# Performance work log

Measured on AMD Instinct MI355X. Metric: run time of the kernel, lower is better.

The kernel has to match this reference:

```python
import jax, jax.numpy as jnp
import numpy as np
from jax import lax

STRIDE = 2
PADDING = 2
KERNEL = 5


def _conv_transpose3d(x, weight, bias):
    # weight: [C_in, C_out, kd, kh, kw] (PyTorch ConvTranspose3d layout)
    # Equivalent dense conv: flip kernel spatially, swap in/out channels,
    # lhs_dilation=stride, symmetric padding = dilation*(k-1) - padding.
    w_t = jnp.flip(weight, axis=(2, 3, 4)).transpose(1, 0, 2, 3, 4)  # [C_out, C_in, k,k,k]
    pad = KERNEL - 1 - PADDING  # = 2
    y = lax.conv_general_dilated(
        x, w_t,
        window_strides=(1, 1, 1),
        padding=[(pad, pad)] * 3,
        lhs_dilation=(STRIDE, STRIDE, STRIDE),
        dimension_numbers=("NCDHW", "OIDHW", "NCDHW"),
    )
    return y + bias[None, :, None, None, None]


def _maxpool3d(y, k):
    # PyTorch MaxPool3d(kernel=k) -> stride=k, no padding, floor mode == VALID
    win = (1, 1, k, k, k)
    return lax.reduce_window(y, -jnp.inf, lax.max, win, win, "VALID")


def setup_inputs() -> dict:
    key = jax.random.key(0)
    k1, k2, k3 = jax.random.split(key, 3)
    x = jax.random.normal(k1, (16, 32, 16, 32, 32), dtype=jnp.float32)
    weight = jax.random.normal(k2, (32, 64, 5, 5, 5), dtype=jnp.float32) * 0.05
    bias = jax.random.normal(k3, (64,), dtype=jnp.float32) * 0.05
    return {"x": x, "weight": weight, "bias": bias}


def reference(x, weight, bias):
    y = _conv_transpose3d(x, weight, bias)     # [16, 64, 31, 63, 63]
    y = _maxpool3d(y, 2)                       # [16, 64, 15, 31, 31]
    y = _maxpool3d(y, 3)                       # [16, 64, 5, 10, 10]
    return jnp.sum(y, axis=1, keepdims=True)   # [16, 1, 5, 10, 10]
```

## Files before the change

### kernel.cpp

```cpp
#include <hip/hip_runtime.h>
#include <hip/hip_bf16.h>
#include <math.h>

typedef short bf16x8 __attribute__((ext_vector_type(8)));
typedef float f32x4 __attribute__((ext_vector_type(4)));

constexpr int CIN = 32, COUT = 64, D = 16, H = 32, W = 32;

constexpr size_t WS_NEED = 884736u;

static __device__ const unsigned char IT_CODE[24] = {
    0, 8, 16, 3,
    1, 9, 17, 11, 19, 7,
    2, 10, 18, 5, 13, 21, 15,
    4, 12, 20, 6, 14, 22, 23};
static __device__ const unsigned char IT_START[5] = {0, 4, 10, 17, 24};
static __device__ const unsigned char EPI_START[10] = {0, 1, 3, 5, 6, 7, 9, 11, 12, 13};
static __device__ const unsigned char EPI_CNT[10]   = {1, 2, 2, 1, 1, 2, 2, 1, 1, 2};

__global__ void prep_w(const float* __restrict__ w, unsigned short* __restrict__ wtp) {
    int idx = blockIdx.x * 256 + threadIdx.x;
    int ci  = idx & 31;
    int co  = (idx >> 5) & 63;
    int tt  = idx >> 11;
    int t   = tt % 27, cls = tt / 27;
    int td = t / 9, th = (t / 3) % 3, tw = t % 3;
    int pd = (cls >> 2) & 1, ph = (cls >> 1) & 1, pw = cls & 1;
    int kd = pd + 2 * td, kh = ph + 2 * th, kw = pw + 2 * tw;
    float v = 0.f;
    if (kd < 5 && kh < 5 && kw < 5)
        v = w[(ci * COUT + co) * 125 + kd * 25 + kh * 5 + kw];
    __hip_bfloat16 b = __float2bfloat16(v);
    wtp[idx] = *reinterpret_cast<unsigned short*>(&b);
}

__device__ __forceinline__ int lpA(int wrow, int quad) {
    return wrow * 64 + ((quad ^ ((wrow >> 1) & 3)) << 4);
}

__global__ __launch_bounds__(256, 2) void main_k(
    const unsigned short* __restrict__ wtp, const float* __restrict__ x,
    const float* __restrict__ bias, float* __restrict__ out)
{
    __shared__ unsigned short Xs[25600];
    int bx = blockIdx.x;
    int h0 = bx % 10;
    int d0 = (bx / 10) % 5;
    int n  = bx / 50;
    int tid = threadIdx.x;

    int id0 = 3 * d0 - 1, ih0 = 3 * h0 - 1;
    for (int u = tid; u < 6400; u += 256) {
        int q  = u & 7;
        int ci = (u >> 3) & 31;
        int p  = u >> 8;
        int dd = p / 5, hl = p % 5;
        int id = id0 + dd, ih = ih0 + hl;
        float4 v = {0.f, 0.f, 0.f, 0.f};
        if (id >= 0 && ih >= 0)
            v = ((const float4*)(x + (((size_t)(n * CIN + ci) * D + id) * H + ih) * W))[q];
        unsigned short hj[4];
        {
            __hip_bfloat16 b0 = __float2bfloat16(v.x); hj[0] = *reinterpret_cast<unsigned short*>(&b0);
            __hip_bfloat16 b1 = __float2bfloat16(v.y); hj[1] = *reinterpret_cast<unsigned short*>(&b1);
            __hip_bfloat16 b2 = __float2bfloat16(v.z); hj[2] = *reinterpret_cast<unsigned short*>(&b2);
            __hip_bfloat16 b3 = __float2bfloat16(v.w); hj[3] = *reinterpret_cast<unsigned short*>(&b3);
        }
        int rowb = p * 1024;
        int cig = ci >> 3, cil = ci & 7;
#pragma unroll
        for (int j = 0; j < 4; ++j) {
            int ww = 4 * q + 1 + j;
            if (ww < 32)
                Xs[rowb + ww * 32 + ((cig ^ ((ww >> 1) & 3)) << 3) + cil] = hj[j];
        }
        if (q == 0)
            Xs[rowb + (cig << 3) + cil] = 0;
    }

    int lane = tid & 63, wv = tid >> 6;
    int l15 = lane & 15, quad = lane >> 4;
    int wv_s = __builtin_amdgcn_readfirstlane(wv);

    int laneB = l15 * 64 + quad * 16;
    int m1 = 16 + l15; if (m1 > 29) m1 = 29;
    int lp00 = lpA(l15 + 0, quad), lp01 = lpA(l15 + 1, quad), lp02 = lpA(l15 + 2, quad);
    int lp10 = lpA(m1 + 0, quad),  lp11 = lpA(m1 + 1, quad),  lp12 = lpA(m1 + 2, quad);

    f32x4 mx[2][4];
#pragma unroll
    for (int mt = 0; mt < 2; ++mt)
#pragma unroll
        for (int nt = 0; nt < 4; ++nt) mx[mt][nt] = (f32x4){-INFINITY, -INFINITY, -INFINITY, -INFINITY};

    __syncthreads();
    const char* xsb = (const char*)Xs;

    int it0 = IT_START[wv_s], it1 = IT_START[wv_s + 1];
#pragma unroll 1
    for (int ii = it0; ii < it1; ++ii) {
        int code  = __builtin_amdgcn_readfirstlane(IT_CODE[ii]);
        int cls   = code & 7;
        int alpha = code >> 3;
        int ntd = 3 - ((cls >> 2) & 1), nth = 3 - ((cls >> 1) & 1), ntw = 3 - (cls & 1);
        const char* tbb = (const char*)wtp + (size_t)cls * 27 * 4096 + laneB;
        const int T = ntd * nth * ntw;

        f32x4 acc[3][2][4];
#pragma unroll
        for (int b = 0; b < 3; ++b)
#pragma unroll
            for (int mt = 0; mt < 2; ++mt)
#pragma unroll
                for (int nt = 0; nt < 4; ++nt) acc[b][mt][nt] = (f32x4){0.f, 0.f, 0.f, 0.f};

        int ptd = 0, pth = 0, ptw = 0;
        auto adv = [&]() {
            ++ptw;
            if (ptw == ntw) { ptw = 0; ++pth; if (pth == nth) { pth = 0; ++ptd; } }
        };

        bf16x8 bE0, bE1, bE2, bE3, aE0, aE1, aE2, aE3, aE4, aE5;
        {
            int Qb = ((alpha + 2) * 5 + 2) * 2048;
            bE0 = *(const bf16x8*)(tbb);
            bE1 = *(const bf16x8*)(tbb + 1024);
            bE2 = *(const bf16x8*)(tbb + 2048);
            bE3 = *(const bf16x8*)(tbb + 3072);
            const char* rb = xsb + Qb;
            aE0 = *(const bf16x8*)(rb + lp02);
            aE1 = *(const bf16x8*)(rb + lp12);
            aE2 = *(const bf16x8*)(rb + 2048 + lp02);
            aE3 = *(const bf16x8*)(rb + 2048 + lp12);
            aE4 = *(const bf16x8*)(rb + 4096 + lp02);
            aE5 = *(const bf16x8*)(rb + 4096 + lp12);
        }
        adv();
        bf16x8 bO0, bO1, bO2, bO3, aO0, aO1, aO2, aO3, aO4, aO5;
        {
            int Qb = ((alpha + 2 - ptd) * 5 + (2 - pth)) * 2048;
            int ss = 2 - ptw;
            const char* bq = tbb + (ptd * 9 + pth * 3 + ptw) * 4096;
            bO0 = *(const bf16x8*)(bq);
            bO1 = *(const bf16x8*)(bq + 1024);
            bO2 = *(const bf16x8*)(bq + 2048);
            bO3 = *(const bf16x8*)(bq + 3072);
            int lpa = ss == 0 ? lp00 : (ss == 1 ? lp01 : lp02);
            int lpb = ss == 0 ? lp10 : (ss == 1 ? lp11 : lp12);
            const char* rb = xsb + Qb;
            aO0 = *(const bf16x8*)(rb + lpa);
            aO1 = *(const bf16x8*)(rb + lpb);
            aO2 = *(const bf16x8*)(rb + 2048 + lpa);
            aO3 = *(const bf16x8*)(rb + 2048 + lpb);
            aO4 = *(const bf16x8*)(rb + 4096 + lpa);
            aO5 = *(const bf16x8*)(rb + 4096 + lpb);
        }
        adv();

#pragma unroll 1
        for (int it = 0; it < T; it += 2) {
            acc[0][0][0] = __builtin_amdgcn_mfma_f32_16x16x32_bf16(aE0, bE0, acc[0][0][0], 0, 0, 0);
            acc[0][0][1] = __builtin_amdgcn_mfma_f32_16x16x32_bf16(aE0, bE1, acc[0][0][1], 0, 0, 0);
            acc[0][0][2] = __builtin_amdgcn_mfma_f32_16x16x32_bf16(aE0, bE2, acc[0][0][2], 0, 0, 0);
            acc[0][0][3] = __builtin_amdgcn_mfma_f32_16x16x32_bf16(aE0, bE3, acc[0][0][3], 0, 0, 0);
            acc[0][1][0] = __builtin_amdgcn_mfma_f32_16x16x32_bf16(aE1, bE0, acc[0][1][0], 0, 0, 0);
            acc[0][1][1] = __builtin_amdgcn_mfma_f32_16x16x32_bf16(aE1, bE1, acc[0][1][1], 0, 0, 0);
            acc[0][1][2] = __builtin_amdgcn_mfma_f32_16x16x32_bf16(aE1, bE2, acc[0][1][2], 0, 0, 0);
            acc[0][1][3] = __builtin_amdgcn_mfma_f32_16x16x32_bf16(aE1, bE3, acc[0][1][3], 0, 0, 0);
            acc[1][0][0] = __builtin_amdgcn_mfma_f32_16x16x32_bf16(aE2, bE0, acc[1][0][0], 0, 0, 0);
            acc[1][0][1] = __builtin_amdgcn_mfma_f32_16x16x32_bf16(aE2, bE1, acc[1][0][1], 0, 0, 0);
            acc[1][0][2] = __builtin_amdgcn_mfma_f32_16x16x32_bf16(aE2, bE2, acc[1][0][2], 0, 0, 0);
            acc[1][0][3] = __builtin_amdgcn_mfma_f32_16x16x32_bf16(aE2, bE3, acc[1][0][3], 0, 0, 0);
            acc[1][1][0] = __builtin_amdgcn_mfma_f32_16x16x32_bf16(aE3, bE0, acc[1][1][0], 0, 0, 0);
            acc[1][1][1] = __builtin_amdgcn_mfma_f32_16x16x32_bf16(aE3, bE1, acc[1][1][1], 0, 0, 0);
            acc[1][1][2] = __builtin_amdgcn_mfma_f32_16x16x32_bf16(aE3, bE2, acc[1][1][2], 0, 0, 0);
            acc[1][1][3] = __builtin_amdgcn_mfma_f32_16x16x32_bf16(aE3, bE3, acc[1][1][3], 0, 0, 0);
            acc[2][0][0] = __builtin_amdgcn_mfma_f32_16x16x32_bf16(aE4, bE0, acc[2][0][0], 0, 0, 0);
            acc[2][0][1] = __builtin_amdgcn_mfma_f32_16x16x32_bf16(aE4, bE1, acc[2][0][1], 0, 0, 0);
            acc[2][0][2] = __builtin_amdgcn_mfma_f32_16x16x32_bf16(aE4, bE2, acc[2][0][2], 0, 0, 0);
            acc[2][0][3] = __builtin_amdgcn_mfma_f32_16x16x32_bf16(aE4, bE3, acc[2][0][3], 0, 0, 0);
            acc[2][1][0] = __builtin_amdgcn_mfma_f32_16x16x32_bf16(aE5, bE0, acc[2][1][0], 0, 0, 0);
            acc[2][1][1] = __builtin_amdgcn_mfma_f32_16x16x32_bf16(aE5, bE1, acc[2][1][1], 0, 0, 0);
            acc[2][1][2] = __builtin_amdgcn_mfma_f32_16x16x32_bf16(aE5, bE2, acc[2][1][2], 0, 0, 0);
            acc[2][1][3] = __builtin_amdgcn_mfma_f32_16x16x32_bf16(aE5, bE3, acc[2][1][3], 0, 0, 0);
            if (it + 2 < T) {
                int Qb = ((alpha + 2 - ptd) * 5 + (2 - pth)) * 2048;
                int ss = 2 - ptw;
                const char* bq = tbb + (ptd * 9 + pth * 3 + ptw) * 4096;
                bE0 = *(const bf16x8*)(bq);
                bE1 = *(const bf16x8*)(bq + 1024);
                bE2 = *(const bf16x8*)(bq + 2048);
                bE3 = *(const bf16x8*)(bq + 3072);
                int lpa = ss == 0 ? lp00 : (ss == 1 ? lp01 : lp02);
                int lpb = ss == 0 ? lp10 : (ss == 1 ? lp11 : lp12);
                const char* rb = xsb + Qb;
                aE0 = *(const bf16x8*)(rb + lpa);
                aE1 = *(const bf16x8*)(rb + lpb);
                aE2 = *(const bf16x8*)(rb + 2048 + lpa);
                aE3 = *(const bf16x8*)(rb + 2048 + lpb);
                aE4 = *(const bf16x8*)(rb + 4096 + lpa);
                aE5 = *(const bf16x8*)(rb + 4096 + lpb);
                adv();
            }
            if (it + 1 < T) {
                acc[0][0][0] = __builtin_amdgcn_mfma_f32_16x16x32_bf16(aO0, bO0, acc[0][0][0], 0, 0, 0);
                acc[0][0][1] = __builtin_amdgcn_mfma_f32_16x16x32_bf16(aO0, bO1, acc[0][0][1], 0, 0, 0);
                acc[0][0][2] = __builtin_amdgcn_mfma_f32_16x16x32_bf16(aO0, bO2, acc[0][0][2], 0, 0, 0);
                acc[0][0][3] = __builtin_amdgcn_mfma_f32_16x16x32_bf16(aO0, bO3, acc[0][0][3], 0, 0, 0);
                acc[0][1][0] = __builtin_amdgcn_mfma_f32_16x16x32_bf16(aO1, bO0, acc[0][1][0], 0, 0, 0);
                acc[0][1][1] = __builtin_amdgcn_mfma_f32_16x16x32_bf16(aO1, bO1, acc[0][1][1], 0, 0, 0);
                acc[0][1][2] = __builtin_amdgcn_mfma_f32_16x16x32_bf16(aO1, bO2, acc[0][1][2], 0, 0, 0);
                acc[0][1][3] = __builtin_amdgcn_mfma_f32_16x16x32_bf16(aO1, bO3, acc[0][1][3], 0, 0, 0);
                acc[1][0][0] = __builtin_amdgcn_mfma_f32_16x16x32_bf16(aO2, bO0, acc[1][0][0], 0, 0, 0);
                acc[1][0][1] = __builtin_amdgcn_mfma_f32_16x16x32_bf16(aO2, bO1, acc[1][0][1], 0, 0, 0);
                acc[1][0][2] = __builtin_amdgcn_mfma_f32_16x16x32_bf16(aO2, bO2, acc[1][0][2], 0, 0, 0);
                acc[1][0][3] = __builtin_amdgcn_mfma_f32_16x16x32_bf16(aO2, bO3, acc[1][0][3], 0, 0, 0);
                acc[1][1][0] = __builtin_amdgcn_mfma_f32_16x16x32_bf16(aO3, bO0, acc[1][1][0], 0, 0, 0);
                acc[1][1][1] = __builtin_amdgcn_mfma_f32_16x16x32_bf16(aO3, bO1, acc[1][1][1], 0, 0, 0);
                acc[1][1][2] = __builtin_amdgcn_mfma_f32_16x16x32_bf16(aO3, bO2, acc[1][1][2], 0, 0, 0);
                acc[1][1][3] = __builtin_amdgcn_mfma_f32_16x16x32_bf16(aO3, bO3, acc[1][1][3], 0, 0, 0);
                acc[2][0][0] = __builtin_amdgcn_mfma_f32_16x16x32_bf16(aO4, bO0, acc[2][0][0], 0, 0, 0);
                acc[2][0][1] = __builtin_amdgcn_mfma_f32_16x16x32_bf16(aO4, bO1, acc[2][0][1], 0, 0, 0);
                acc[2][0][2] = __builtin_amdgcn_mfma_f32_16x16x32_bf16(aO4, bO2, acc[2][0][2], 0, 0, 0);
                acc[2][0][3] = __builtin_amdgcn_mfma_f32_16x16x32_bf16(aO4, bO3, acc[2][0][3], 0, 0, 0);
                acc[2][1][0] = __builtin_amdgcn_mfma_f32_16x16x32_bf16(aO5, bO0, acc[2][1][0], 0, 0, 0);
                acc[2][1][1] = __builtin_amdgcn_mfma_f32_16x16x32_bf16(aO5, bO1, acc[2][1][1], 0, 0, 0);
                acc[2][1][2] = __builtin_amdgcn_mfma_f32_16x16x32_bf16(aO5, bO2, acc[2][1][2], 0, 0, 0);
                acc[2][1][3] = __builtin_amdgcn_mfma_f32_16x16x32_bf16(aO5, bO3, acc[2][1][3], 0, 0, 0);
                if (it + 3 < T) {
                    int Qb = ((alpha + 2 - ptd) * 5 + (2 - pth)) * 2048;
                    int ss = 2 - ptw;
                    const char* bq = tbb + (ptd * 9 + pth * 3 + ptw) * 4096;
                    bO0 = *(const bf16x8*)(bq);
                    bO1 = *(const bf16x8*)(bq + 1024);
                    bO2 = *(const bf16x8*)(bq + 2048);
                    bO3 = *(const bf16x8*)(bq + 3072);
                    int lpa = ss == 0 ? lp00 : (ss == 1 ? lp01 : lp02);
                    int lpb = ss == 0 ? lp10 : (ss == 1 ? lp11 : lp12);
                    const char* rb = xsb + Qb;
                    aO0 = *(const bf16x8*)(rb + lpa);
                    aO1 = *(const bf16x8*)(rb + lpb);
                    aO2 = *(const bf16x8*)(rb + 2048 + lpa);
                    aO3 = *(const bf16x8*)(rb + 2048 + lpb);
                    aO4 = *(const bf16x8*)(rb + 4096 + lpa);
                    aO5 = *(const bf16x8*)(rb + 4096 + lpb);
                    adv();
                }
            }
        }

#pragma unroll
        for (int mt = 0; mt < 2; ++mt)
#pragma unroll
            for (int nt = 0; nt < 4; ++nt)
#pragma unroll
                for (int r = 0; r < 4; ++r) {
                    float m = fmaxf(fmaxf(acc[0][mt][nt][r], acc[1][mt][nt][r]), acc[2][mt][nt][r]);
                    mx[mt][nt][r] = fmaxf(mx[mt][nt][r], m);
                }
    }

    __syncthreads();
    float* epi = (float*)Xs;
    int fsm0 = (0x3123 >> (quad * 4)) & 15;
    int fsm1 = (0x4312 >> (quad * 4)) & 15;
#pragma unroll
    for (int mt = 0; mt < 2; ++mt) {
        int fs = mt ? fsm1 : fsm0;
        int g  = mt * 4 + quad;
#pragma unroll
        for (int nt = 0; nt < 4; ++nt) {
            float a0 = mx[mt][nt][0], a1 = mx[mt][nt][1], a2 = mx[mt][nt][2], a3 = mx[mt][nt][3];
            float t01 = fmaxf(a0, a1), t012 = fmaxf(t01, a2), t0123 = fmaxf(t012, a3);
            float pA = fs == 1 ? a0 : (fs == 2 ? t01 : (fs == 3 ? t012 : t0123));
            float t23 = fmaxf(a2, a3), t123 = fmaxf(a1, t23);
            float pB = fs == 1 ? t123 : (fs == 2 ? t23 : (fs == 3 ? a3 : -INFINITY));
            epi[((wv * 8 + g) * 2 + 0) * 64 + nt * 16 + l15] = pA;
            epi[((wv * 8 + g) * 2 + 1) * 64 + nt * 16 + l15] = pB;
        }
    }
    __syncthreads();

    int elemBase = ((n * 5 + d0) * 10 + h0) * 10;
    float bco = bias[lane];
#pragma unroll 1
    for (int win = wv_s; win < 10; win += 4) {
        int st = EPI_START[win], cnt = EPI_CNT[win];
        float v = -INFINITY;
        for (int src = 0; src < 4; ++src)
            for (int e = st; e < st + cnt; ++e)
                v = fmaxf(v, epi[(src * 16 + e) * 64 + lane]);
        v += bco;
#pragma unroll
        for (int off = 32; off > 0; off >>= 1) v += __shfl_xor(v, off);
        if (lane == 0) out[elemBase + win] = v;
    }
}

__global__ __launch_bounds__(256) void fused_fallback(
    const float* __restrict__ x, const float* __restrict__ wsrc,
    const float* __restrict__ bias, float* __restrict__ out)
{
    __shared__ float xs[CIN * 125];
    __shared__ float wmax[4][64];
    const int b  = blockIdx.x;
    const int w0 = b % 10, h0 = (b / 10) % 10, d0 = (b / 100) % 5, n = b / 500;
    const int tid = threadIdx.x;
    const int id0 = 3 * d0 - 1, ih0 = 3 * h0 - 1, iw0 = 3 * w0 - 1;
    for (int e = tid; e < CIN * 125; e += 256) {
        int kk = e % 5, jj = (e / 5) % 5, ii = (e / 25) % 5, c = e / 125;
        int id = id0 + ii, ih = ih0 + jj, iw = iw0 + kk;
        float v = 0.f;
        if (id >= 0 && ih >= 0 && iw >= 0)
            v = x[(((n * CIN + c) * D + id) * H + ih) * W + iw];
        xs[e] = v;
    }
    __syncthreads();
    const int lane = tid & 63, wv = tid >> 6;
    float lmax = -INFINITY;
    for (int ccls = 0; ccls < 2; ++ccls) {
        const int cls = wv * 2 + ccls;
        const int pd = (cls >> 2) & 1, ph = (cls >> 1) & 1, pw = cls & 1;
        float acc[27];
#pragma unroll
        for (int i = 0; i < 27; ++i) acc[i] = 0.f;
        for (int ci = 0; ci < CIN; ++ci) {
            float wr[27];
#pragma unroll
            for (int t = 0; t < 27; ++t) {
                int td = t / 9, th = (t / 3) % 3, tw = t % 3;
                int kd = pd + 2 * td, kh = ph + 2 * th, kw = pw + 2 * tw;
                wr[t] = (kd < 5 && kh < 5 && kw < 5)
                          ? wsrc[((ci * 64 + lane) * 125) + kd * 25 + kh * 5 + kw] : 0.f;
            }
            const float* xb = xs + ci * 125;
#pragma unroll
            for (int td = 0; td < 3; ++td)
#pragma unroll
            for (int th = 0; th < 3; ++th)
#pragma unroll
            for (int tw = 0; tw < 3; ++tw) {
                const float wval = wr[(td * 3 + th) * 3 + tw];
#pragma unroll
                for (int a = 0; a < 3; ++a)
#pragma unroll
                for (int bb = 0; bb < 3; ++bb)
#pragma unroll
                for (int cc = 0; cc < 3; ++cc)
                    acc[(a * 3 + bb) * 3 + cc] +=
                        xb[(a + 2 - td) * 25 + (bb + 2 - th) * 5 + (cc + 2 - tw)] * wval;
            }
        }
#pragma unroll
        for (int i = 0; i < 27; ++i) lmax = fmaxf(lmax, acc[i]);
    }
    wmax[wv][lane] = lmax;
    __syncthreads();
    if (wv == 0) {
        float m = fmaxf(fmaxf(wmax[0][lane], wmax[1][lane]),
                        fmaxf(wmax[2][lane], wmax[3][lane]));
        m += bias[lane];
        for (int off = 32; off > 0; off >>= 1) m += __shfl_down(m, off);
        if (lane == 0) out[b] = m;
    }
}

extern "C" void kernel_launch(void* const* d_in, const int* in_sizes, int n_in,
                              void* d_out, int out_size, void* d_ws, size_t ws_size,
                              hipStream_t stream) {
    const float* x    = (const float*)d_in[0];
    const float* w    = (const float*)d_in[1];
    const float* bias = (const float*)d_in[2];
    float* out = (float*)d_out;

    if (ws_size >= WS_NEED) {
        unsigned short* wtp = (unsigned short*)d_ws;
        prep_w<<<1728, 256, 0, stream>>>(w, wtp);
        main_k<<<800, 256, 0, stream>>>(wtp, x, bias, out);
    } else {
        fused_fallback<<<8000, 256, 0, stream>>>(x, w, bias, out);
    }
}
```

Before: 201.7 us.

## Split each output row tile into two W-halves across blocks, raising occupancy

Each block now computes half of the output W range (one 16-row M tile instead of two), doubling the grid to 1600 blocks. Accumulator and A-fragment register use roughly halves, which allows launch bounds of 3 waves per SIMD, and the fold into partial pool windows moves into the per-iteration loop. It also adds s_setprio around MFMA bursts. The cost is reloading overlapping x halo and all weights per half-block, plus extra staging work.

Result: slower. 243.0 us (+20.5%).

```diff
diff --git a/kernel.cpp b/kernel.cpp
--- a/kernel.cpp
+++ b/kernel.cpp
@@ -15,8 +15,8 @@
     2, 10, 18, 5, 13, 21, 15,
     4, 12, 20, 6, 14, 22, 23};
 static __device__ const unsigned char IT_START[5] = {0, 4, 10, 17, 24};
-static __device__ const unsigned char EPI_START[10] = {0, 1, 3, 5, 6, 7, 9, 11, 12, 13};
-static __device__ const unsigned char EPI_CNT[10]   = {1, 2, 2, 1, 1, 2, 2, 1, 1, 2};
+static __device__ const unsigned char EPI_START[5] = {0, 1, 3, 5, 6};
+static __device__ const unsigned char EPI_CNT[5]   = {1, 2, 2, 1, 1};
 
 __global__ void prep_w(const float* __restrict__ w, unsigned short* __restrict__ wtp) {
     int idx = blockIdx.x * 256 + threadIdx.x;
@@ -38,22 +38,27 @@
     return wrow * 64 + ((quad ^ ((wrow >> 1) & 3)) << 4);
 }
 
-__global__ __launch_bounds__(256, 2) void main_k(
+__global__ __launch_bounds__(256, 3) void main_k(
     const unsigned short* __restrict__ wtp, const float* __restrict__ x,
     const float* __restrict__ bias, float* __restrict__ out)
 {
     __shared__ unsigned short Xs[25600];
-    int bx = blockIdx.x;
-    int h0 = bx % 10;
-    int d0 = (bx / 10) % 5;
-    int n  = bx / 50;
+    int bx   = blockIdx.x;
+    int half = bx & 1;
+    int obx  = bx >> 1;
+    int h0 = obx % 10;
+    int d0 = (obx / 10) % 5;
+    int n  = obx / 50;
     int tid = threadIdx.x;
 
     int id0 = 3 * d0 - 1, ih0 = 3 * h0 - 1;
-    for (int u = tid; u < 6400; u += 256) {
-        int q  = u & 7;
-        int ci = (u >> 3) & 31;
-        int p  = u >> 8;
+    int qb = half ? 3 : 0;
+    for (int u = tid; u < 4000; u += 256) {
+        int qi = u % 5;
+        int t2 = u / 5;
+        int ci = t2 & 31;
+        int p  = t2 >> 5;
+        int q  = qb + qi;
         int dd = p / 5, hl = p % 5;
         int id = id0 + dd, ih = ih0 + hl;
         float4 v = {0.f, 0.f, 0.f, 0.f};
@@ -83,18 +88,19 @@
     int wv_s = __builtin_amdgcn_readfirstlane(wv);
 
     int laneB = l15 * 64 + quad * 16;
-    int m1 = 16 + l15; if (m1 > 29) m1 = 29;
-    int lp00 = lpA(l15 + 0, quad), lp01 = lpA(l15 + 1, quad), lp02 = lpA(l15 + 2, quad);
-    int lp10 = lpA(m1 + 0, quad),  lp11 = lpA(m1 + 1, quad),  lp12 = lpA(m1 + 2, quad);
-
-    f32x4 mx[2][4];
-#pragma unroll
-    for (int mt = 0; mt < 2; ++mt)
-#pragma unroll
-        for (int nt = 0; nt < 4; ++nt) mx[mt][nt] = (f32x4){-INFINITY, -INFINITY, -INFINITY, -INFINITY};
+    int mtmp = 15 + l15;
+    int mb = half ? (mtmp > 29 ? 29 : mtmp) : l15;
+    int lp0 = lpA(mb + 0, quad), lp1 = lpA(mb + 1, quad), lp2 = lpA(mb + 2, quad);
+
+    float mxp[4][2];
+#pragma unroll
+    for (int nt = 0; nt < 4; ++nt) { mxp[nt][0] = -INFINITY; mxp[nt][1] = -INFINITY; }
 
     __syncthreads();
     const char* xsb = (const char*)Xs;
+
+    int fsm = half ? 0x4123 : 0x3123;
+    int fs  = (fsm >> (quad * 4)) & 15;
 
     int it0 = IT_START[wv_s], it1 = IT_START[wv_s + 1];
 #pragma unroll 1
@@ -106,13 +112,11 @@
         const char* tbb = (const char*)wtp + (size_t)cls * 27 * 4096 + laneB;
         const int T = ntd * nth * ntw;
 
-        f32x4 acc[3][2][4];
+        f32x4 acc[3][4];
 #pragma unroll
         for (int b = 0; b < 3; ++b)
 #pragma unroll
-            for (int mt = 0; mt < 2; ++mt)
-#pragma unroll
-                for (int nt = 0; nt < 4; ++nt) acc[b][mt][nt] = (f32x4){0.f, 0.f, 0.f, 0.f};
+            for (int nt = 0; nt < 4; ++nt) acc[b][nt] = (f32x4){0.f, 0.f, 0.f, 0.f};
 
         int ptd = 0, pth = 0, ptw = 0;
         auto adv = [&]() {
@@ -120,7 +124,7 @@
             if (ptw == ntw) { ptw = 0; ++pth; if (pth == nth) { pth = 0; ++ptd; } }
         };
 
-        bf16x8 bE0, bE1, bE2, bE3, aE0, aE1, aE2, aE3, aE4, aE5;
+        bf16x8 bE0, bE1, bE2, bE3, aE0, aE1, aE2;
         {
             int Qb = ((alpha + 2) * 5 + 2) * 2048;
             bE0 = *(const bf16x8*)(tbb);
@@ -128,15 +132,12 @@
             bE2 = *(const bf16x8*)(tbb + 2048);
             bE3 = *(const bf16x8*)(tbb + 3072);
             const char* rb = xsb + Qb;
-            aE0 = *(const bf16x8*)(rb + lp02);
-            aE1 = *(const bf16x8*)(rb + lp12);
-            aE2 = *(const bf16x8*)(rb + 2048 + lp02);
-            aE3 = *(const bf16x8*)(rb + 2048 + lp12);
-            aE4 = *(const bf16x8*)(rb + 4096 + lp02);
-            aE5 = *(const bf16x8*)(rb + 4096 + lp12);
+            aE0 = *(const bf16x8*)(rb + lp2);
+            aE1 = *(const bf16x8*)(rb + 2048 + lp2);
+            aE2 = *(const bf16x8*)(rb + 4096 + lp2);
         }
         adv();
-        bf16x8 bO0, bO1, bO2, bO3, aO0, aO1, aO2, aO3, aO4, aO5;
+        bf16x8 bO0, bO1, bO2, bO3, aO0, aO1, aO2;
         {
             int Qb = ((alpha + 2 - ptd) * 5 + (2 - pth)) * 2048;
             int ss = 2 - ptw;
@@ -145,44 +146,30 @@
             bO1 = *(const bf16x8*)(bq + 1024);
             bO2 = *(const bf16x8*)(bq + 2048);
             bO3 = *(const bf16x8*)(bq + 3072);
-            int lpa = ss == 0 ? lp00 : (ss == 1 ? lp01 : lp02);
-            int lpb = ss == 0 ? lp10 : (ss == 1 ? lp11 : lp12);
+            int lpx = ss == 0 ? lp0 : (ss == 1 ? lp1 : lp2);
             const char* rb = xsb + Qb;
-            aO0 = *(const bf16x8*)(rb + lpa);
-            aO1 = *(const bf16x8*)(rb + lpb);
-            aO2 = *(const bf16x8*)(rb + 2048 + lpa);
-            aO3 = *(const bf16x8*)(rb + 2048 + lpb);
-            aO4 = *(const bf16x8*)(rb + 4096 + lpa);
-            aO5 = *(const bf16x8*)(rb + 4096 + lpb);
+            aO0 = *(const bf16x8*)(rb + lpx);
+            aO1 = *(const bf16x8*)(rb + 2048 + lpx);
+            aO2 = *(const bf16x8*)(rb + 4096 + lpx);
         }
         adv();
 
 #pragma unroll 1
         for (int it = 0; it < T; it += 2) {
-            acc[0][0][0] = __builtin_amdgcn_mfma_f32_16x16x32_bf16(aE0, bE0, acc[0][0][0], 0, 0, 0);
-            acc[0][0][1] = __builtin_amdgcn_mfma_f32_16x16x32_bf16(aE0, bE1, acc[0][0][1], 0, 0, 0);
-            acc[0][0][2] = __builtin_amdgcn_mfma_f32_16x16x32_bf16(aE0, bE2, acc[0][0][2], 0, 0, 0);
-            acc[0][0][3] = __builtin_amdgcn_mfma_f32_16x16x32_bf16(aE0, bE3, acc[0][0][3], 0, 0, 0);
-            acc[0][1][0] = __builtin_amdgcn_mfma_f32_16x16x32_bf16(aE1, bE0, acc[0][1][0], 0, 0, 0);
-            acc[0][1][1] = __builtin_amdgcn_mfma_f32_16x16x32_bf16(aE1, bE1, acc[0][1][1], 0, 0, 0);
-            acc[0][1][2] = __builtin_amdgcn_mfma_f32_16x16x32_bf16(aE1, bE2, acc[0][1][2], 0, 0, 0);
-            acc[0][1][3] = __builtin_amdgcn_mfma_f32_16x16x32_bf16(aE1, bE3, acc[0][1][3], 0, 0, 0);
-            acc[1][0][0] = __builtin_amdgcn_mfma_f32_16x16x32_bf16(aE2, bE0, acc[1][0][0], 0, 0, 0);
-            acc[1][0][1] = __builtin_amdgcn_mfma_f32_16x16x32_bf16(aE2, bE1, acc[1][0][1], 0, 0, 0);
-            acc[1][0][2] = __builtin_amdgcn_mfma_f32_16x16x32_bf16(aE2, bE2, acc[1][0][2], 0, 0, 0);
-            acc[1][0][3] = __builtin_amdgcn_mfma_f32_16x16x32_bf16(aE2, bE3, acc[1][0][3], 0, 0, 0);
-            acc[1][1][0] = __builtin_amdgcn_mfma_f32_16x16x32_bf16(aE3, bE0, acc[1][1][0], 0, 0, 0);
-            acc[1][1][1] = __builtin_amdgcn_mfma_f32_16x16x32_bf16(aE3, bE1, acc[1][1][1], 0, 0, 0);
-            acc[1][1][2] = __builtin_amdgcn_mfma_f32_16x16x32_bf16(aE3, bE2, acc[1][1][2], 0, 0, 0);
-            acc[1][1][3] = __builtin_amdgcn_mfma_f32_16x16x32_bf16(aE3, bE3, acc[1][1][3], 0, 0, 0);
-            acc[2][0][0] = __builtin_amdgcn_mfma_f32_16x16x32_bf16(aE4, bE0, acc[2][0][0], 0, 0, 0);
-            acc[2][0][1] = __builtin_amdgcn_mfma_f32_16x16x32_bf16(aE4, bE1, acc[2][0][1], 0, 0, 0);
-            acc[2][0][2] = __builtin_amdgcn_mfma_f32_16x16x32_bf16(aE4, bE2, acc[2][0][2], 0, 0, 0);
-            acc[2][0][3] = __builtin_amdgcn_mfma_f32_16x16x32_bf16(aE4, bE3, acc[2][0][3], 0, 0, 0);
-            acc[2][1][0] = __builtin_amdgcn_mfma_f32_16x16x32_bf16(aE5, bE0, acc[2][1][0], 0, 0, 0);
-            acc[2][1][1] = __builtin_amdgcn_mfma_f32_16x16x32_bf16(aE5, bE1, acc[2][1][1], 0, 0, 0);
-            acc[2][1][2] = __builtin_amdgcn_mfma_f32_16x16x32_bf16(aE5, bE2, acc[2][1][2], 0, 0, 0);
-            acc[2][1][3] = __builtin_amdgcn_mfma_f32_16x16x32_bf16(aE5, bE3, acc[2][1][3], 0, 0, 0);
+            __builtin_amdgcn_s_setprio(1);
+            acc[0][0] = __builtin_amdgcn_mfma_f32_16x16x32_bf16(aE0, bE0, acc[0][0], 0, 0, 0);
+            acc[0][1] = __builtin_amdgcn_mfma_f32_16x16x32_bf16(aE0, bE1, acc[0][1], 0, 0, 0);
+            acc[0][2] = __builtin_amdgcn_mfma_f32_16x16x32_bf16(aE0, bE2, acc[0][2], 0, 0, 0);
+            acc[0][3] = __builtin_amdgcn_mfma_f32_16x16x32_bf16(aE0, bE3, acc[0][3], 0, 0, 0);
+            acc[1][0] = __builtin_amdgcn_mfma_f32_16x16x32_bf16(aE1, bE0, acc[1][0], 0, 0, 0);
+            acc[1][1] = __builtin_amdgcn_mfma_f32_16x16x32_bf16(aE1, bE1, acc[1][1], 0, 0, 0);
+            acc[1][2] = __builtin_amdgcn_mfma_f32_16x16x32_bf16(aE1, bE2, acc[1][2], 0, 0, 0);
+            acc[1][3] = __builtin_amdgcn_mfma_f32_16x16x32_bf16(aE1, bE3, acc[1][3], 0, 0, 0);
+            acc[2][0] = __builtin_amdgcn_mfma_f32_16x16x32_bf16(aE2, bE0, acc[2][0], 0, 0, 0);
+            acc[2][1] = __builtin_amdgcn_mfma_f32_16x16x32_bf16(aE2, bE1, acc[2][1], 0, 0, 0);
+            acc[2][2] = __builtin_amdgcn_mfma_f32_16x16x32_bf16(aE2, bE2, acc[2][2], 0, 0, 0);
+            acc[2][3] = __builtin_amdgcn_mfma_f32_16x16x32_bf16(aE2, bE3, acc[2][3], 0, 0, 0);
+            __builtin_amdgcn_s_setprio(0);
             if (it + 2 < T) {
                 int Qb = ((alpha + 2 - ptd) * 5 + (2 - pth)) * 2048;
                 int ss = 2 - ptw;
@@ -191,42 +178,28 @@
                 bE1 = *(const bf16x8*)(bq + 1024);
                 bE2 = *(const bf16x8*)(bq + 2048);
                 bE3 = *(const bf16x8*)(bq + 3072);
-                int lpa = ss == 0 ? lp00 : (ss == 1 ? lp01 : lp02);
-                int lpb = ss == 0 ? lp10 : (ss == 1 ? lp11 : lp12);
+                int lpx = ss == 0 ? lp0 : (ss == 1 ? lp1 : lp2);
                 const char* rb = xsb + Qb;
-                aE0 = *(const bf16x8*)(rb + lpa);
-                aE1 = *(const bf16x8*)(rb + lpb);
-                aE2 = *(const bf16x8*)(rb + 2048 + lpa);
-                aE3 = *(const bf16x8*)(rb + 2048 + lpb);
-                aE4 = *(const bf16x8*)(rb + 4096 + lpa);
-                aE5 = *(const bf16x8*)(rb + 4096 + lpb);
+                aE0 = *(const bf16x8*)(rb + lpx);
+                aE1 = *(const bf16x8*)(rb + 2048 + lpx);
+                aE2 = *(const bf16x8*)(rb + 4096 + lpx);
                 adv();
             }
             if (it + 1 < T) {
-                acc[0][0][0] = __builtin_amdgcn_mfma_f32_16x16x32_bf16(aO0, bO0, acc[0][0][0], 0, 0, 0);
-                acc[0][0][1] = __builtin_amdgcn_mfma_f32_16x16x32_bf16(aO0, bO1, acc[0][0][1], 0, 0, 0);
-                acc[0][0][2] = __builtin_amdgcn_mfma_f32_16x16x32_bf16(aO0, bO2, acc[0][0][2], 0, 0, 0);
-                acc[0][0][3] = __builtin_amdgcn_mfma_f32_16x16x32_bf16(aO0, bO3, acc[0][0][3], 0, 0, 0);
-                acc[0][1][0] = __builtin_amdgcn_mfma_f32_16x16x32_bf16(aO1, bO0, acc[0][1][0], 0, 0, 0);
-                acc[0][1][1] = __builtin_amdgcn_mfma_f32_16x16x32_bf16(aO1, bO1, acc[0][1][1], 0, 0, 0);
-                acc[0][1][2] = __builtin_amdgcn_mfma_f32_16x16x32_bf16(aO1, bO2, acc[0][1][2], 0, 0, 0);
-                acc[0][1][3] = __builtin_amdgcn_mfma_f32_16x16x32_bf16(aO1, bO3, acc[0][1][3], 0, 0, 0);
-                acc[1][0][0] = __builtin_amdgcn_mfma_f32_16x16x32_bf16(aO2, bO0, acc[1][0][0], 0, 0, 0);
-                acc[1][0][1] = __builtin_amdgcn_mfma_f32_16x16x32_bf16(aO2, bO1, acc[1][0][1], 0, 0, 0);
-                acc[1][0][2] = __builtin_amdgcn_mfma_f32_16x16x32_bf16(aO2, bO2, acc[1][0][2], 0, 0, 0);
-                acc[1][0][3] = __builtin_amdgcn_mfma_f32_16x16x32_bf16(aO2, bO3, acc[1][0][3], 0, 0, 0);
-                acc[1][1][0] = __builtin_amdgcn_mfma_f32_16x16x32_bf16(aO3, bO0, acc[1][1][0], 0, 0, 0);
-                acc[1][1][1] = __builtin_amdgcn_mfma_f32_16x16x32_bf16(aO3, bO1, acc[1][1][1], 0, 0, 0);
-                acc[1][1][2] = __builtin_amdgcn_mfma_f32_16x16x32_bf16(aO3, bO2, acc[1][1][2], 0, 0, 0);
-                acc[1][1][3] = __builtin_amdgcn_mfma_f32_16x16x32_bf16(aO3, bO3, acc[1][1][3], 0, 0, 0);
-                acc[2][0][0] = __builtin_amdgcn_mfma_f32_16x16x32_bf16(aO4, bO0, acc[2][0][0], 0, 0, 0);
-                acc[2][0][1] = __builtin_amdgcn_mfma_f32_16x16x32_bf16(aO4, bO1, acc[2][0][1], 0, 0, 0);
-                acc[2][0][2] = __builtin_amdgcn_mfma_f32_16x16x32_bf16(aO4, bO2, acc[2][0][2], 0, 0, 0);
-                acc[2][0][3] = __builtin_amdgcn_mfma_f32_16x16x32_bf16(aO4, bO3, acc[2][0][3], 0, 0, 0);
-                acc[2][1][0] = __builtin_amdgcn_mfma_f32_16x16x32_bf16(aO5, bO0, acc[2][1][0], 0, 0, 0);
-                acc[2][1][1] = __builtin_amdgcn_mfma_f32_16x16x32_bf16(aO5, bO1, acc[2][1][1], 0, 0, 0);
-                acc[2][1][2] = __builtin_amdgcn_mfma_f32_16x16x32_bf16(aO5, bO2, acc[2][1][2], 0, 0, 0);
-                acc[2][1][3] = __builtin_amdgcn_mfma_f32_16x16x32_bf16(aO5, bO3, acc[2][1][3], 0, 0, 0);
+                __builtin_amdgcn_s_setprio(1);
+                acc[0][0] = __builtin_amdgcn_mfma_f32_16x16x32_bf16(aO0, bO0, acc[0][0], 0, 0, 0);
+                acc[0][1] = __builtin_amdgcn_mfma_f32_16x16x32_bf16(aO0, bO1, acc[0][1], 0, 0, 0);
+                acc[0][2] = __builtin_amdgcn_mfma_f32_16x16x32_bf16(aO0, bO2, acc[0][2], 0, 0, 0);
+                acc[0][3] = __builtin_amdgcn_mfma_f32_16x16x32_bf16(aO0, bO3, acc[0][3], 0, 0, 0);
+                acc[1][0] = __builtin_amdgcn_mfma_f32_16x16x32_bf16(aO1, bO0, acc[1][0], 0, 0, 0);
+                acc[1][1] = __builtin_amdgcn_mfma_f32_16x16x32_bf16(aO1, bO1, acc[1][1], 0, 0, 0);
+                acc[1][2] = __builtin_amdgcn_mfma_f32_16x16x32_bf16(aO1, bO2, acc[1][2], 0, 0, 0);
+                acc[1][3] = __builtin_amdgcn_mfma_f32_16x16x32_bf16(aO1, bO3, acc[1][3], 0, 0, 0);
+                acc[2][0] = __builtin_amdgcn_mfma_f32_16x16x32_bf16(aO2, bO0, acc[2][0], 0, 0, 0);
+                acc[2][1] = __builtin_amdgcn_mfma_f32_16x16x32_bf16(aO2, bO1, acc[2][1], 0, 0, 0);
+                acc[2][2] = __builtin_amdgcn_mfma_f32_16x16x32_bf16(aO2, bO2, acc[2][2], 0, 0, 0);
+                acc[2][3] = __builtin_amdgcn_mfma_f32_16x16x32_bf16(aO2, bO3, acc[2][3], 0, 0, 0);
+                __builtin_amdgcn_s_setprio(0);
                 if (it + 3 < T) {
                     int Qb = ((alpha + 2 - ptd) * 5 + (2 - pth)) * 2048;
                     int ss = 2 - ptw;
@@ -235,65 +208,53 @@
                     bO1 = *(const bf16x8*)(bq + 1024);
                     bO2 = *(const bf16x8*)(bq + 2048);
                     bO3 = *(const bf16x8*)(bq + 3072);
-                    int lpa = ss == 0 ? lp00 : (ss == 1 ? lp01 : lp02);
-                    int lpb = ss == 0 ? lp10 : (ss == 1 ? lp11 : lp12);
+                    int lpx = ss == 0 ? lp0 : (ss == 1 ? lp1 : lp2);
                     const char* rb = xsb + Qb;
-                    aO0 = *(const bf16x8*)(rb + lpa);
-                    aO1 = *(const bf16x8*)(rb + lpb);
-                    aO2 = *(const bf16x8*)(rb + 2048 + lpa);
-                    aO3 = *(const bf16x8*)(rb + 2048 + lpb);
-                    aO4 = *(const bf16x8*)(rb + 4096 + lpa);
-                    aO5 = *(const bf16x8*)(rb + 4096 + lpb);
+                    aO0 = *(const bf16x8*)(rb + lpx);
+                    aO1 = *(const bf16x8*)(rb + 2048 + lpx);
+                    aO2 = *(const bf16x8*)(rb + 4096 + lpx);
                     adv();
                 }
             }
         }
 
 #pragma unroll
-        for (int mt = 0; mt < 2; ++mt)
-#pragma unroll
-            for (int nt = 0; nt < 4; ++nt)
-#pragma unroll
-                for (int r = 0; r < 4; ++r) {
-                    float m = fmaxf(fmaxf(acc[0][mt][nt][r], acc[1][mt][nt][r]), acc[2][mt][nt][r]);
-                    mx[mt][nt][r] = fmaxf(mx[mt][nt][r], m);
-                }
+        for (int nt = 0; nt < 4; ++nt) {
+            float r0 = fmaxf(fmaxf(acc[0][nt][0], acc[1][nt][0]), acc[2][nt][0]);
+            float r1 = fmaxf(fmaxf(acc[0][nt][1], acc[1][nt][1]), acc[2][nt][1]);
+            float r2 = fmaxf(fmaxf(acc[0][nt][2], acc[1][nt][2]), acc[2][nt][2]);
+            float r3 = fmaxf(fmaxf(acc[0][nt][3], acc[1][nt][3]), acc[2][nt][3]);
+            float t01 = fmaxf(r0, r1), t012 = fmaxf(t01, r2), t0123 = fmaxf(t012, r3);
+            float pA = fs == 1 ? r0 : (fs == 2 ? t01 : (fs == 3 ? t012 : t0123));
+            float t23 = fmaxf(r2, r3), t123 = fmaxf(r1, t23);
+            float pB = fs == 1 ? t123 : (fs == 2 ? t23 : (fs == 3 ? r3 : -INFINITY));
+            mxp[nt][0] = fmaxf(mxp[nt][0], pA);
+            mxp[nt][1] = fmaxf(mxp[nt][1], pB);
+        }
     }
 
     __syncthreads();
     float* epi = (float*)Xs;
-    int fsm0 = (0x3123 >> (quad * 4)) & 15;
-    int fsm1 = (0x4312 >> (quad * 4)) & 15;
-#pragma unroll
-    for (int mt = 0; mt < 2; ++mt) {
-        int fs = mt ? fsm1 : fsm0;
-        int g  = mt * 4 + quad;
-#pragma unroll
-        for (int nt = 0; nt < 4; ++nt) {
-            float a0 = mx[mt][nt][0], a1 = mx[mt][nt][1], a2 = mx[mt][nt][2], a3 = mx[mt][nt][3];
-            float t01 = fmaxf(a0, a1), t012 = fmaxf(t01, a2), t0123 = fmaxf(t012, a3);
-            float pA = fs == 1 ? a0 : (fs == 2 ? t01 : (fs == 3 ? t012 : t0123));
-            float t23 = fmaxf(a2, a3), t123 = fmaxf(a1, t23);
-            float pB = fs == 1 ? t123 : (fs == 2 ? t23 : (fs == 3 ? a3 : -INFINITY));
-            epi[((wv * 8 + g) * 2 + 0) * 64 + nt * 16 + l15] = pA;
-            epi[((wv * 8 + g) * 2 + 1) * 64 + nt * 16 + l15] = pB;
-        }
-    }
-    __syncthreads();
-
-    int elemBase = ((n * 5 + d0) * 10 + h0) * 10;
+#pragma unroll
+    for (int nt = 0; nt < 4; ++nt) {
+        epi[(wv * 8 + quad * 2 + 0) * 64 + nt * 16 + l15] = mxp[nt][0];
+        epi[(wv * 8 + quad * 2 + 1) * 64 + nt * 16 + l15] = mxp[nt][1];
+    }
+    __syncthreads();
+
+    int elemBase = ((n * 5 + d0) * 10 + h0) * 10 + half * 5;
     float bco = bias[lane];
 #pragma unroll 1
-    for (int win = wv_s; win < 10; win += 4) {
-        int st = EPI_START[win], cnt = EPI_CNT[win];
+    for (int winl = wv_s; winl < 5; winl += 4) {
+        int st = EPI_START[winl], cnt = EPI_CNT[winl];
         float v = -INFINITY;
         for (int src = 0; src < 4; ++src)
             for (int e = st; e < st + cnt; ++e)
-                v = fmaxf(v, epi[(src * 16 + e) * 64 + lane]);
+                v = fmaxf(v, epi[(src * 8 + e) * 64 + lane]);
         v += bco;
 #pragma unroll
         for (int off = 32; off > 0; off >>= 1) v += __shfl_xor(v, off);
-        if (lane == 0) out[elemBase + win] = v;
+        if (lane == 0) out[elemBase + winl] = v;
     }
 }
 
@@ -376,7 +337,7 @@
     if (ws_size >= WS_NEED) {
         unsigned short* wtp = (unsigned short*)d_ws;
         prep_w<<<1728, 256, 0, stream>>>(w, wtp);
-        main_k<<<800, 256, 0, stream>>>(wtp, x, bias, out);
+        main_k<<<1600, 256, 0, stream>>>(wtp, x, bias, out);
     } else {
         fused_fallback<<<8000, 256, 0, stream>>>(x, w, bias, out);
     }
```
